# Kernel tuning notes

Hardware: AMD Instinct MI355X
Metric: run time of the kernel (lower is better)

## Reference

```python
import jax, jax.numpy as jnp
import numpy as np

B, S, H, R = 2, 4096, 2048, 2048
NB, CW = 16, 4
BW = R // NB


def _block_diag_linear(x, w, b):
    # x: [B,S,R]; w: [NB,BW,BW]; b: [NB,BW]
    xb = x.reshape(x.shape[0], x.shape[1], NB, BW)
    out = jnp.einsum('bsni,nij->bsnj', xb, w) + b
    return out.reshape(x.shape)


def _causal_conv1d(x, conv_w, conv_b):
    # depthwise causal temporal conv: out[t] = sum_i w[i]*x[t-CW+1+i] + b
    xp = jnp.pad(x, ((0, 0), (CW - 1, 0), (0, 0)))
    out = conv_b
    for i in range(CW):
        out = out + conv_w[i] * xp[:, i:i + x.shape[1], :]
    return out


def _rg_lru_scan(x, x_gate_pre, a_gate_pre, a_param):
    gate_x = jax.nn.sigmoid(x_gate_pre)
    gate_a = jax.nn.sigmoid(a_gate_pre)
    log_a = -8.0 * gate_a * jax.nn.softplus(a_param)  # [B,S,R]
    a = jnp.exp(log_a)
    multiplier = jnp.sqrt(-jnp.expm1(2.0 * log_a))  # sqrt(1 - a^2)
    norm_x = x * gate_x * multiplier
    # h_t = a_t * h_{t-1} + norm_x_t via parallel associative scan over time
    def combine(c1, c2):
        a1, b1 = c1
        a2, b2 = c2
        return a1 * a2, a2 * b1 + b2
    _, h = jax.lax.associative_scan(combine, (a, norm_x), axis=1)
    return h


def setup_inputs() -> dict:
    key = jax.random.key(0)
    ks = jax.random.split(key, 9)
    x = jax.random.normal(ks[0], (B, S, H), dtype=jnp.float32)
    W_xy = jax.random.normal(ks[1], (2 * R, H), dtype=jnp.float32) / np.sqrt(H)
    ig_w = jax.random.normal(ks[2], (NB, BW, BW), dtype=jnp.float32) / np.sqrt(BW)
    ig_b = jnp.zeros((NB, BW), dtype=jnp.float32)
    ag_w = jax.random.normal(ks[3], (NB, BW, BW), dtype=jnp.float32) / np.sqrt(BW)
    ag_b = jnp.zeros((NB, BW), dtype=jnp.float32)
    # forget_init: a = a_real in [0.9, 0.999]; a_param = softplus^{-1}(-log(a_real))
    unif = jax.random.uniform(ks[4], (R,), dtype=jnp.float32)
    a_real = 0.5 * jnp.log(unif * (0.999 ** 2 - 0.9 ** 2) + 0.9 ** 2 + 1e-8)
    a_param = jnp.log(jnp.expm1(-a_real))
    conv_w = jax.random.normal(ks[5], (CW, R), dtype=jnp.float32) / np.sqrt(CW * R)
    conv_b = jnp.zeros((R,), dtype=jnp.float32)
    # resid_proj is zero-init in the module; use small random so output is non-trivial
    W_resid = 0.02 * jax.random.normal(ks[6], (H, R), dtype=jnp.float32)
    return {"x": x, "W_xy": W_xy, "ig_w": ig_w, "ig_b": ig_b,
            "ag_w": ag_w, "ag_b": ag_b, "a_param": a_param,
            "conv_w": conv_w, "conv_b": conv_b, "W_resid": W_resid}


def reference(x, W_xy, ig_w, ig_b, ag_w, ag_b, a_param, conv_w, conv_b, W_resid):
    xy = jnp.einsum('bsh,rh->bsr', x, W_xy)  # [B,S,2R]
    xr, y = jnp.split(xy, 2, axis=-1)
    xc = _causal_conv1d(xr, conv_w, conv_b)
    x_gate_pre = _block_diag_linear(xc, ig_w, ig_b)
    a_gate_pre = _block_diag_linear(xc, ag_w, ag_b)
    h = _rg_lru_scan(xc, x_gate_pre, a_gate_pre, a_param)
    out = jnp.einsum('bsr,hr->bsh', jax.nn.gelu(y, approximate=False) * h, W_resid)
    return out
```

## Files before the change

kernel.cpp:

```cpp
#include <hip/hip_runtime.h>
#include <hip/hip_bf16.h>

typedef __hip_bfloat16 bf16;
typedef __attribute__((ext_vector_type(8))) short s16x8;
typedef __attribute__((ext_vector_type(4))) float f32x4;

#define B_ 2
#define S_ 4096
#define H_ 2048
#define R_ 2048
#define M_ 8192
#define NB_ 16
#define BW_ 128
#define CHUNK 64
#define NCH 64

__device__ __forceinline__ short f2b_s(float f) {
    return (short)__builtin_bit_cast(unsigned short, __float2bfloat16(f));
}
__device__ __forceinline__ float b2f_s(short s) {
    unsigned int u = ((unsigned int)(unsigned short)s) << 16;
    return __builtin_bit_cast(float, u);
}
__device__ __forceinline__ float sigm_fast(float x) { return 1.f / (1.f + __expf(-x)); }

__device__ __forceinline__ void async_g2l(const void* g, void* l) {
    __builtin_amdgcn_global_load_lds((const __attribute__((address_space(1))) void*)g,
                                     (__attribute__((address_space(3))) void*)l, 16, 0, 0);
}

__global__ __launch_bounds__(256) void cast_all(const float* __restrict__ x,
                                                const float* __restrict__ wxy,
                                                const float* __restrict__ wres,
                                                const float* __restrict__ igw,
                                                const float* __restrict__ agw,
                                                const float* __restrict__ apar,
                                                bf16* __restrict__ xbf,
                                                bf16* __restrict__ wxyb,
                                                bf16* __restrict__ wresb,
                                                bf16* __restrict__ wT,
                                                float* __restrict__ sp8) {
    __shared__ float tile[32 * 129];
    int blk = blockIdx.x;
    int tid = threadIdx.x;
    if (blk >= 14336) {
        int b2 = blk - 14336;
        if (b2 == 32) {
#pragma unroll
            for (int it = 0; it < 8; ++it) {
                int r = it * 256 + tid;
                float ap = apar[r];
                sp8[r] = 8.f * (ap > 20.f ? ap : log1pf(expf(ap)));
            }
            return;
        }
        int p = b2 >> 4, n = b2 & 15;
        const float* w = (p ? agw : igw) + (size_t)n * 16384;
        bf16* o = wT + (size_t)b2 * 16384;
        for (int s = 0; s < 4; ++s) {
#pragma unroll
            for (int it = 0; it < 16; ++it) {
                int u = it * 256 + tid;
                tile[(u >> 7) * 129 + (u & 127)] = w[(s * 32 + (u >> 7)) * 128 + (u & 127)];
            }
            __syncthreads();
#pragma unroll
            for (int it = 0; it < 16; ++it) {
                int v = it * 256 + tid;
                int j = v >> 5, ii = v & 31;
                o[j * 128 + s * 32 + ii] = __float2bfloat16(tile[ii * 129 + j]);
            }
            __syncthreads();
        }
        return;
    }
    int idx = blk * 256 + tid;
    const float* in; bf16* out; int off;
    if (idx < 2097152)      { in = x;    out = xbf;   off = idx; }
    else if (idx < 3145728) { in = wxy;  out = wxyb;  off = idx - 2097152; }
    else                    { in = wres; out = wresb; off = idx - 3145728; }
    size_t i8 = (size_t)off * 8;
    float4 v0 = *(const float4*)(in + i8);
    float4 v1 = *(const float4*)(in + i8 + 4);
    s16x8 o;
    o[0] = f2b_s(v0.x); o[1] = f2b_s(v0.y); o[2] = f2b_s(v0.z); o[3] = f2b_s(v0.w);
    o[4] = f2b_s(v1.x); o[5] = f2b_s(v1.y); o[6] = f2b_s(v1.z); o[7] = f2b_s(v1.w);
    *(s16x8*)(out + i8) = o;
}

__device__ __forceinline__ void store_c(float* p, float v) { *p = v; }
__device__ __forceinline__ void store_c(bf16* p, float v) { *p = __float2bfloat16(v); }

template <typename OutT>
__global__ __launch_bounds__(256, 4) void gemm_bt(const bf16* __restrict__ A,
                                                  const bf16* __restrict__ Bm,
                                                  OutT* __restrict__ C,
                                                  int K, int lda, int ldb, int ldc,
                                                  int gelu_from) {
    __shared__ __align__(16) short As[128 * 64];
    __shared__ __align__(16) short Bs[128 * 64];
    const int tid = threadIdx.x;
    const int lane = tid & 63, wave = tid >> 6;
    const int waveM = wave >> 1, waveN = wave & 1;
    const int mBase = blockIdx.y * 128, nBase = blockIdx.x * 128;
    const int fm = lane & 15, q = lane >> 4;
    const bool dog = (nBase >= gelu_from);

    f32x4 acc[4][4];
#pragma unroll
    for (int i = 0; i < 4; ++i)
#pragma unroll
        for (int j = 0; j < 4; ++j) acc[i][j] = (f32x4){0.f, 0.f, 0.f, 0.f};

    for (int k0 = 0; k0 < K; k0 += 64) {
        __syncthreads();
#pragma unroll
        for (int it = 0; it < 4; ++it) {
            int off = it * 4096 + tid * 16;
            int r = off >> 7;
            int g = ((off & 127) >> 4) ^ (r & 7);
            async_g2l(A + (size_t)(mBase + r) * lda + k0 + g * 8, (char*)As + off);
            async_g2l(Bm + (size_t)(nBase + r) * ldb + k0 + g * 8, (char*)Bs + off);
        }
        __syncthreads();
#pragma unroll
        for (int s = 0; s < 2; ++s) {
            s16x8 af[4], bfr[4];
#pragma unroll
            for (int i = 0; i < 4; ++i) {
                int row = waveM * 64 + i * 16 + fm;
                af[i] = *(const s16x8*)((char*)As + row * 128 + ((((s << 2) + q) ^ (row & 7)) << 4));
                int col = waveN * 64 + i * 16 + fm;
                bfr[i] = *(const s16x8*)((char*)Bs + col * 128 + ((((s << 2) + q) ^ (col & 7)) << 4));
            }
#pragma unroll
            for (int i = 0; i < 4; ++i)
#pragma unroll
                for (int j = 0; j < 4; ++j)
                    acc[i][j] = __builtin_amdgcn_mfma_f32_16x16x32_bf16(af[i], bfr[j], acc[i][j], 0, 0, 0);
        }
    }
#pragma unroll
    for (int i = 0; i < 4; ++i) {
        int rowg = mBase + waveM * 64 + i * 16 + q * 4;
#pragma unroll
        for (int j = 0; j < 4; ++j) {
            int colg = nBase + waveN * 64 + j * 16 + fm;
#pragma unroll
            for (int rr = 0; rr < 4; ++rr) {
                float v = acc[i][j][rr];
                if (dog) v = 0.5f * v * (1.f + erff(v * 0.70710678f));
                store_c(C + (size_t)(rowg + rr) * ldc + colg, v);
            }
        }
    }
}

__global__ __launch_bounds__(256) void gate_kernel(const bf16* __restrict__ xy,
                                                   const float* __restrict__ cw,
                                                   const float* __restrict__ cb,
                                                   const bf16* __restrict__ wT,
                                                   const float* __restrict__ igb,
                                                   const float* __restrict__ agb,
                                                   const float* __restrict__ sp8,
                                                   bf16* __restrict__ hloc_out,
                                                   bf16* __restrict__ cum_out,
                                                   float2* __restrict__ AH) {
    __shared__ __align__(16) short As[64 * 128];
    __shared__ __align__(16) char  Wmem[128 * 256];
    short* Xs   = (short*)Wmem;
    short* Ws   = (short*)Wmem;
    float* a_sh = (float*)Wmem;
    const int n = blockIdx.x;
    const int mBase = blockIdx.y * 64;
    const int tid = threadIdx.x;
    const int lane = tid & 63, wave = tid >> 6;
    const int fm = lane & 15, q = lane >> 4;
    const int t0 = mBase & (S_ - 1);

#pragma unroll
    for (int it = 0; it < 5; ++it) {
        int u = it * 256 + tid;
        if (u < 67 * 16) {
            int rr = u >> 4, gg = u & 15;
            s16x8 v = (s16x8){0, 0, 0, 0, 0, 0, 0, 0};
            if (t0 != 0 || rr >= 3) {
                int m = mBase + rr - 3;
                v = *(const s16x8*)(xy + (size_t)m * 4096 + n * BW_ + gg * 8);
            }
            *(s16x8*)((char*)Xs + u * 16) = v;
        }
    }
    __syncthreads();

    {
        int col = tid & 127, rh = tid >> 7;
        int rbase = n * BW_ + col;
        float w0c = cw[rbase], w1c = cw[R_ + rbase], w2c = cw[2 * R_ + rbase],
              w3c = cw[3 * R_ + rbase];
        float bc = cb[rbase];
        int r0 = rh * 32;
        float xm3 = b2f_s(Xs[(r0 + 0) * 128 + col]);
        float xm2 = b2f_s(Xs[(r0 + 1) * 128 + col]);
        float xm1 = b2f_s(Xs[(r0 + 2) * 128 + col]);
#pragma unroll
        for (int rw = 0; rw < 32; ++rw) {
            int row = r0 + rw;
            float x0 = b2f_s(Xs[(row + 3) * 128 + col]);
            float v = bc + w0c * xm3 + w1c * xm2 + w2c * xm1 + w3c * x0;
            xm3 = xm2; xm2 = xm1; xm1 = x0;
            *(short*)((char*)As + row * 256 + ((((col >> 3)) ^ (row & 15)) << 4) +
                      (col & 7) * 2) = f2b_s(v);
        }
    }
    __syncthreads();

    const bf16* w0 = wT + (size_t)n * 16384;
#pragma unroll
    for (int it = 0; it < 8; ++it) {
        int off = it * 4096 + tid * 16;
        int j = off >> 8;
        int g = ((off & 255) >> 4) ^ (j & 15);
        async_g2l(w0 + j * 128 + g * 8, (char*)Ws + off);
    }
    __syncthreads();

    f32x4 accI[8], accA[8];
#pragma unroll
    for (int jj = 0; jj < 8; ++jj) {
        accI[jj] = (f32x4){0.f, 0.f, 0.f, 0.f};
        accA[jj] = (f32x4){0.f, 0.f, 0.f, 0.f};
    }

    const int row = wave * 16 + fm;
#pragma unroll
    for (int s = 0; s < 4; ++s) {
        s16x8 af = *(const s16x8*)((char*)As + row * 256 + ((((s << 2) + q) ^ (row & 15)) << 4));
#pragma unroll
        for (int jj = 0; jj < 8; ++jj) {
            int wrow = jj * 16 + fm;
            s16x8 bw = *(const s16x8*)((char*)Ws + wrow * 256 + ((((s << 2) + q) ^ (wrow & 15)) << 4));
            accI[jj] = __builtin_amdgcn_mfma_f32_16x16x32_bf16(af, bw, accI[jj], 0, 0, 0);
        }
    }
    __syncthreads();
    const bf16* w1 = wT + (size_t)(NB_ + n) * 16384;
#pragma unroll
    for (int it = 0; it < 8; ++it) {
        int off = it * 4096 + tid * 16;
        int j = off >> 8;
        int g = ((off & 255) >> 4) ^ (j & 15);
        async_g2l(w1 + j * 128 + g * 8, (char*)Ws + off);
    }
    __syncthreads();
#pragma unroll
    for (int s = 0; s < 4; ++s) {
        s16x8 af = *(const s16x8*)((char*)As + row * 256 + ((((s << 2) + q) ^ (row & 15)) << 4));
#pragma unroll
        for (int jj = 0; jj < 8; ++jj) {
            int wrow = jj * 16 + fm;
            s16x8 bw = *(const s16x8*)((char*)Ws + wrow * 256 + ((((s << 2) + q) ^ (wrow & 15)) << 4));
            accA[jj] = __builtin_amdgcn_mfma_f32_16x16x32_bf16(af, bw, accA[jj], 0, 0, 0);
        }
    }
    __syncthreads();

#pragma unroll
    for (int jj = 0; jj < 8; ++jj) {
        int col = jj * 16 + fm;
        int r = n * BW_ + col;
        float bi = igb[r], ba = agb[r];
        float s8 = sp8[r];
#pragma unroll
        for (int rr = 0; rr < 4; ++rr) {
            int rowl = wave * 16 + q * 4 + rr;
            short* slot = (short*)((char*)As + rowl * 256 +
                          ((((col >> 3)) ^ (rowl & 15)) << 4) + (col & 7) * 2);
            float xcv = b2f_s(*slot);
            float xg = accI[jj][rr] + bi;
            float ag = accA[jj][rr] + ba;
            float la = -s8 * sigm_fast(ag);
            float av = __expf(la);
            float t2 = 2.f * la;
            float nem = (t2 > -0.125f)
                ? -t2 * (1.f + t2 * (0.5f + t2 * (0.16666667f + t2 * 0.04166667f)))
                : 1.f - av * av;
            float nxv = xcv * sigm_fast(xg) * sqrtf(nem);
            short nxs = f2b_s(nxv);
            a_sh[rowl * 128 + col] = av;
            *slot = nxs;
        }
    }
    __syncthreads();

    if (tid < 128) {
        int col = tid;
        float h = 0.f, cum = 1.f;
#pragma unroll 4
        for (int t = 0; t < CHUNK; ++t) {
            short* slot = (short*)((char*)As + t * 256 +
                          ((((col >> 3)) ^ (t & 15)) << 4) + (col & 7) * 2);
            float a = a_sh[t * 128 + col];
            float nxv = b2f_s(*slot);
            h = fmaf(a, h, nxv);
            cum *= a;
            *slot = f2b_s(h);
            a_sh[t * 128 + col] = cum;
        }
        int b = mBase >> 12, c = (mBase & (S_ - 1)) >> 6;
        int so = ((b * NCH + c) << 11) + n * BW_ + col;
        AH[so] = make_float2(cum, h);
    }
    __syncthreads();

#pragma unroll
    for (int it = 0; it < 4; ++it) {
        int u = it * 256 + tid;
        int t = u >> 4, gg = u & 15;
        s16x8 hv = *(const s16x8*)((char*)As + t * 256 + ((gg ^ (t & 15)) << 4));
        s16x8 cv;
#pragma unroll
        for (int i = 0; i < 8; ++i) cv[i] = f2b_s(a_sh[t * 128 + gg * 8 + i]);
        size_t o = (size_t)(mBase + t) * R_ + n * BW_ + gg * 8;
        *(s16x8*)(hloc_out + o) = hv;
        *(s16x8*)(cum_out + o) = cv;
    }
}

__global__ __launch_bounds__(256) void scan_carry(const float2* __restrict__ AH,
                                                  float* __restrict__ carry) {
    int idx = blockIdx.x * 256 + threadIdx.x;
    int r = idx & (R_ - 1), b = idx >> 11;
    int base = b * NCH * R_ + r;
    float cy = 0.f;
    for (int c0 = 0; c0 < NCH; c0 += 8) {
        float2 v[8];
#pragma unroll
        for (int j = 0; j < 8; ++j) v[j] = AH[base + (c0 + j) * R_];
#pragma unroll
        for (int j = 0; j < 8; ++j) {
            carry[base + (c0 + j) * R_] = cy;
            cy = fmaf(v[j].x, cy, v[j].y);
        }
    }
}

__global__ __launch_bounds__(256) void scan_passB(const bf16* __restrict__ hloc,
                                                  const bf16* __restrict__ cum,
                                                  const float* __restrict__ carry,
                                                  const bf16* __restrict__ xy,
                                                  bf16* __restrict__ g_out) {
    int idx = blockIdx.x * 256 + threadIdx.x;
    int m = idx >> 8;
    int r = (idx & 255) << 3;
    int b = m >> 12, c = (m & 4095) >> 6;
    int so = ((b * NCH + c) << 11) + r;
    size_t o = (size_t)m * R_ + r;
    s16x8 hv = *(const s16x8*)(hloc + o);
    s16x8 cv = *(const s16x8*)(cum + o);
    float4 cy0 = *(const float4*)(carry + so);
    float4 cy1 = *(const float4*)(carry + so + 4);
    s16x8 yv = *(const s16x8*)(xy + (size_t)m * 4096 + 2048 + r);
    float cya0 = cy0.x, cya1 = cy0.y, cya2 = cy0.z, cya3 = cy0.w;
    float cya4 = cy1.x, cya5 = cy1.y, cya6 = cy1.z, cya7 = cy1.w;
    s16x8 g;
#pragma unroll 8
    for (int i = 0; i < 8; ++i) {
        float cy = (i == 0) ? cya0 : (i == 1) ? cya1 : (i == 2) ? cya2 : (i == 3) ? cya3
                 : (i == 4) ? cya4 : (i == 5) ? cya5 : (i == 6) ? cya6 : cya7;
        float h = fmaf(b2f_s(cv[i]), cy, b2f_s(hv[i]));
        g[i] = f2b_s(b2f_s(yv[i]) * h);
    }
    *(s16x8*)(g_out + o) = g;
}

extern "C" void kernel_launch(void* const* d_in, const int* in_sizes, int n_in,
                              void* d_out, int out_size, void* d_ws, size_t ws_size,
                              hipStream_t stream) {
    const float* x    = (const float*)d_in[0];
    const float* Wxy  = (const float*)d_in[1];
    const float* igw  = (const float*)d_in[2];
    const float* igb  = (const float*)d_in[3];
    const float* agw  = (const float*)d_in[4];
    const float* agb  = (const float*)d_in[5];
    const float* apar = (const float*)d_in[6];
    const float* cw   = (const float*)d_in[7];
    const float* cb   = (const float*)d_in[8];
    const float* Wres = (const float*)d_in[9];
    float* out = (float*)d_out;

    char* ws = (char*)d_ws;
    const size_t MiB = (size_t)1 << 20;
    bf16*  xbf   = (bf16*)(ws);
    bf16*  hloc  = (bf16*)(ws);
    bf16*  wxyb  = (bf16*)(ws + 32 * MiB);
    float* cyb   = (float*)(ws + 36 * MiB);
    bf16*  xy    = (bf16*)(ws + 48 * MiB);
    bf16*  wresb = (bf16*)(ws + 112 * MiB);
    bf16*  wT    = (bf16*)(ws + 120 * MiB);
    float* sp8   = (float*)(ws + 121 * MiB);
    bf16*  g     = (bf16*)(ws + 120 * MiB);
    bf16*  cum   = (bf16*)(ws + 152 * MiB);
    float2* AH   = (float2*)(ws + 184 * MiB);

    cast_all<<<14369, 256, 0, stream>>>(x, Wxy, Wres, igw, agw, apar,
                                        xbf, wxyb, wresb, wT, sp8);

    gemm_bt<bf16><<<dim3(32, 64), 256, 0, stream>>>(xbf, wxyb, xy,
                                                    2048, 2048, 2048, 4096, 2048);

    gate_kernel<<<dim3(NB_, 128), 256, 0, stream>>>(xy, cw, cb, wT, igb, agb, sp8,
                                                    hloc, cum, AH);

    scan_carry<<<16, 256, 0, stream>>>(AH, cyb);
    scan_passB<<<8192, 256, 0, stream>>>(hloc, cum, cyb, xy, g);

    gemm_bt<float><<<dim3(16, 64), 256, 0, stream>>>(g, wresb, out,
                                                     2048, 2048, 2048, 2048, 1 << 30);
}
```

Baseline: 466.0 us.

## Add pipelined 256x256 MFMA GEMM for output projection and move GELU into scan

Adds a new 512-thread GEMM kernel with 256x256 tiles, double-buffered LDS (128 KiB), interleaved async global-to-LDS staging, explicit waitcnt/barrier phasing and setprio around MFMA bursts. It is used for the final projection to overlap loads with math and raise per-tile reuse. GELU is moved from the first GEMM's epilogue into the scan pass, so the GEMM epilogue no longer branches. The large LDS footprint limits occupancy, and the hand-written wait counts are fragile.

```diff
diff --git a/kernel.cpp b/kernel.cpp
--- a/kernel.cpp
+++ b/kernel.cpp
@@ -95,8 +95,7 @@
 __global__ __launch_bounds__(256, 4) void gemm_bt(const bf16* __restrict__ A,
                                                   const bf16* __restrict__ Bm,
                                                   OutT* __restrict__ C,
-                                                  int K, int lda, int ldb, int ldc,
-                                                  int gelu_from) {
+                                                  int K, int lda, int ldb, int ldc) {
     __shared__ __align__(16) short As[128 * 64];
     __shared__ __align__(16) short Bs[128 * 64];
     const int tid = threadIdx.x;
@@ -104,7 +103,6 @@
     const int waveM = wave >> 1, waveN = wave & 1;
     const int mBase = blockIdx.y * 128, nBase = blockIdx.x * 128;
     const int fm = lane & 15, q = lane >> 4;
-    const bool dog = (nBase >= gelu_from);
 
     f32x4 acc[4][4];
 #pragma unroll
@@ -147,11 +145,125 @@
         for (int j = 0; j < 4; ++j) {
             int colg = nBase + waveN * 64 + j * 16 + fm;
 #pragma unroll
-            for (int rr = 0; rr < 4; ++rr) {
-                float v = acc[i][j][rr];
-                if (dog) v = 0.5f * v * (1.f + erff(v * 0.70710678f));
-                store_c(C + (size_t)(rowg + rr) * ldc + colg, v);
-            }
+            for (int rr = 0; rr < 4; ++rr)
+                store_c(C + (size_t)(rowg + rr) * ldc + colg, acc[i][j][rr]);
+        }
+    }
+}
+
+#define MFMA16(Q)                                                                     \
+    _Pragma("unroll") for (int j = 0; j < 4; ++j) {                                   \
+        acc[2*(Q)][j]   = __builtin_amdgcn_mfma_f32_16x16x32_bf16(af[0][0], bfr[j][0], acc[2*(Q)][j], 0, 0, 0);   \
+        acc[2*(Q)][j]   = __builtin_amdgcn_mfma_f32_16x16x32_bf16(af[0][1], bfr[j][1], acc[2*(Q)][j], 0, 0, 0);   \
+        acc[2*(Q)+1][j] = __builtin_amdgcn_mfma_f32_16x16x32_bf16(af[1][0], bfr[j][0], acc[2*(Q)+1][j], 0, 0, 0); \
+        acc[2*(Q)+1][j] = __builtin_amdgcn_mfma_f32_16x16x32_bf16(af[1][1], bfr[j][1], acc[2*(Q)+1][j], 0, 0, 0); \
+    }
+
+#define PHASE(BASEP, Q, LOADB, STMTS, VMSTMT)                                         \
+    rdA2(BASEP, Q, af);                                                               \
+    if (LOADB) rdB8(BASEP, bfr);                                                      \
+    STMTS;                                                                            \
+    if (LOADB) asm volatile("s_waitcnt lgkmcnt(8)" ::: "memory");                     \
+    __builtin_amdgcn_s_barrier();                                                     \
+    asm volatile("s_waitcnt lgkmcnt(0)" ::: "memory");                                \
+    __builtin_amdgcn_sched_barrier(0);                                                \
+    __builtin_amdgcn_s_setprio(1);                                                    \
+    MFMA16(Q);                                                                        \
+    __builtin_amdgcn_s_setprio(0);                                                    \
+    VMSTMT;                                                                           \
+    __builtin_amdgcn_s_barrier();                                                     \
+    __builtin_amdgcn_sched_barrier(0);
+
+template <typename OutT>
+__global__ __launch_bounds__(512, 2) void gemm256(const bf16* __restrict__ A,
+                                                  const bf16* __restrict__ Bm,
+                                                  OutT* __restrict__ C,
+                                                  int K, int lda, int ldb, int ldc) {
+    extern __shared__ __align__(16) char lds[];
+    const int tid = threadIdx.x;
+    const int lane = tid & 63, wave = tid >> 6;
+    const int wm = wave >> 2, wn = wave & 3;
+    const int fm = lane & 15, q = lane >> 4;
+    const int mBase = blockIdx.y * 256, nBase = blockIdx.x * 256;
+    const int NT = K >> 6, LT = (NT >> 1) - 1;
+
+    auto stage_half = [&](int tile, int hh) {
+        if (tile >= NT) return;
+        const bf16* src = (hh < 2) ? Bm : A;
+        const int ld = (hh < 2) ? ldb : lda;
+        const int rowBase = ((hh < 2) ? nBase : mBase) + ((hh & 1) << 7);
+        char* dst = lds + ((tile & 1) << 16) + ((hh < 2) ? 32768 : 0) + ((hh & 1) << 14);
+#pragma unroll
+        for (int rnd = 0; rnd < 2; ++rnd) {
+            int off = rnd * 8192 + tid * 16;
+            int r = off >> 7;
+            int g = ((off >> 4) & 7) ^ (r & 7);
+            async_g2l(src + (size_t)(rowBase + r) * ld + tile * 64 + g * 8, dst + off);
+        }
+    };
+    auto rdA2 = [&](const char* base, int qp, s16x8 (&dst)[2][2]) {
+#pragma unroll
+        for (int i2 = 0; i2 < 2; ++i2) {
+            int r7 = (qp * 2 + i2) * 16 + fm;
+            const char* p = base + (wm << 14) + r7 * 128;
+#pragma unroll
+            for (int kk = 0; kk < 2; ++kk)
+                dst[i2][kk] = *(const s16x8*)(p + ((((kk << 2) + q) ^ (r7 & 7)) << 4));
+        }
+    };
+    auto rdB8 = [&](const char* base, s16x8 (&dst)[4][2]) {
+#pragma unroll
+        for (int j = 0; j < 4; ++j) {
+            int col = wn * 64 + j * 16 + fm;
+            const char* p = base + 32768 + ((col >> 7) << 14) + (col & 127) * 128;
+#pragma unroll
+            for (int kk = 0; kk < 2; ++kk)
+                dst[j][kk] = *(const s16x8*)(p + ((((kk << 2) + q) ^ (col & 7)) << 4));
+        }
+    };
+
+    s16x8 af[2][2], bfr[4][2];
+    f32x4 acc[8][4];
+#pragma unroll
+    for (int i = 0; i < 8; ++i)
+#pragma unroll
+        for (int j = 0; j < 4; ++j) acc[i][j] = (f32x4){0.f, 0.f, 0.f, 0.f};
+
+    stage_half(0, 0); stage_half(0, 1); stage_half(0, 2); stage_half(0, 3);
+    stage_half(1, 0); stage_half(1, 1);
+    asm volatile("s_waitcnt vmcnt(4)" ::: "memory");
+    __builtin_amdgcn_s_barrier();
+    __builtin_amdgcn_sched_barrier(0);
+
+    for (int t = 0; t <= LT; ++t) {
+        const int Ta = 2 * t, Tb = Ta + 1;
+        const char* b0 = lds;
+        const char* b1 = lds + 65536;
+
+        PHASE(b0, 0, 1, { stage_half(Tb, 2); }, {})
+        PHASE(b0, 1, 0, { stage_half(Tb, 3); stage_half(Ta + 2, 0); }, {})
+        PHASE(b0, 2, 0, { stage_half(Ta + 2, 1); }, {})
+        PHASE(b0, 3, 0, {},
+              { if (t < LT) asm volatile("s_waitcnt vmcnt(4)" ::: "memory");
+                else        asm volatile("s_waitcnt vmcnt(0)" ::: "memory"); })
+
+        PHASE(b1, 0, 1, { stage_half(Ta + 2, 2); }, {})
+        PHASE(b1, 1, 0, { stage_half(Ta + 2, 3); stage_half(Tb + 2, 0); }, {})
+        PHASE(b1, 2, 0, { stage_half(Tb + 2, 1); }, {})
+        PHASE(b1, 3, 0, {},
+              { if (t < LT) asm volatile("s_waitcnt vmcnt(4)" ::: "memory");
+                else        asm volatile("s_waitcnt vmcnt(0)" ::: "memory"); })
+    }
+
+#pragma unroll
+    for (int i = 0; i < 8; ++i) {
+        int rowg = mBase + wm * 128 + i * 16 + q * 4;
+#pragma unroll
+        for (int j = 0; j < 4; ++j) {
+            int colg = nBase + wn * 64 + j * 16 + fm;
+#pragma unroll
+            for (int rr = 0; rr < 4; ++rr)
+                store_c(C + (size_t)(rowg + rr) * ldc + colg, acc[i][j][rr]);
         }
     }
 }
@@ -369,7 +481,9 @@
         float cy = (i == 0) ? cya0 : (i == 1) ? cya1 : (i == 2) ? cya2 : (i == 3) ? cya3
                  : (i == 4) ? cya4 : (i == 5) ? cya5 : (i == 6) ? cya6 : cya7;
         float h = fmaf(b2f_s(cv[i]), cy, b2f_s(hv[i]));
-        g[i] = f2b_s(b2f_s(yv[i]) * h);
+        float y = b2f_s(yv[i]);
+        float gg = 0.5f * y * (1.f + erff(y * 0.70710678f));
+        g[i] = f2b_s(gg * h);
     }
     *(s16x8*)(g_out + o) = g;
 }
@@ -406,8 +520,7 @@
     cast_all<<<14369, 256, 0, stream>>>(x, Wxy, Wres, igw, agw, apar,
                                         xbf, wxyb, wresb, wT, sp8);
 
-    gemm_bt<bf16><<<dim3(32, 64), 256, 0, stream>>>(xbf, wxyb, xy,
-                                                    2048, 2048, 2048, 4096, 2048);
+    gemm_bt<bf16><<<dim3(32, 64), 256, 0, stream>>>(xbf, wxyb, xy, 2048, 2048, 2048, 4096);
 
     gate_kernel<<<dim3(NB_, 128), 256, 0, stream>>>(xy, cw, cb, wT, igb, agb, sp8,
                                                     hloc, cum, AH);
@@ -415,6 +528,6 @@
     scan_carry<<<16, 256, 0, stream>>>(AH, cyb);
     scan_passB<<<8192, 256, 0, stream>>>(hloc, cum, cyb, xy, g);
 
-    gemm_bt<float><<<dim3(16, 64), 256, 0, stream>>>(g, wresb, out,
-                                                     2048, 2048, 2048, 2048, 1 << 30);
-}
+    gemm256<float><<<dim3(8, 32), 512, 131072, stream>>>(g, wresb, out,
+                                                         2048, 2048, 2048, 2048);
+}
```

New measurement: 452.3 us. 1.03x faster.
